# Performance work log

Measured on AMD Instinct MI355X. Metric: run time of the kernel, lower is better.

Reference implementation:

```python
import jax, jax.numpy as jnp
import numpy as np

NUM_HEADS = 6
DIM = 192
WIN = 7  # window_size = (7, 7), n = 49
N = WIN * WIN
TABLE = (2 * WIN - 1) * (2 * WIN - 1)  # 169
SCALE = (DIM // NUM_HEADS) ** (-0.5)


def setup_inputs() -> dict:
    key = jax.random.key(0)
    k1, k2, k3, k4, k5, k6 = jax.random.split(key, 6)
    B_ = 8192   # num_windows * batch = 1024 * 8
    NW = 1024   # windows per image (224/7)^2
    qkv = jax.random.normal(k1, (B_, N, 3 * DIM), dtype=jnp.float32)
    rpi = jax.random.randint(k2, (N, N), 0, TABLE, dtype=jnp.int64)
    # shift-window mask: 0 where attend, -100 where masked (Swin convention)
    mask = jnp.where(jax.random.uniform(k3, (NW, N, N)) < 0.8, 0.0, -100.0).astype(jnp.float32)
    bias_table = 0.02 * jax.random.normal(k4, (TABLE, NUM_HEADS), dtype=jnp.float32)
    proj_w = 0.02 * jax.random.normal(k5, (DIM, DIM), dtype=jnp.float32)
    proj_b = jnp.zeros((DIM,), dtype=jnp.float32)
    return {"qkv": qkv, "rpi": rpi, "mask": mask,
            "bias_table": bias_table, "proj_w": proj_w, "proj_b": proj_b}


def reference(qkv, rpi, mask, bias_table, proj_w, proj_b):
    b_, n, c3 = qkv.shape
    c = c3 // 3
    hd = c // NUM_HEADS
    # (b_, n, 3, h, hd) -> (3, b_, h, n, hd)
    qkv = qkv.reshape(b_, n, 3, NUM_HEADS, hd).transpose(2, 0, 3, 1, 4)
    q, k, v = qkv[0], qkv[1], qkv[2]
    attn = jnp.einsum('bhid,bhjd->bhij', q * SCALE, k)  # (b_, h, n, n)
    # relative position bias gather: (n*n,) -> (n, n, h) -> (h, n, n)
    rpb = bias_table[rpi.reshape(-1)].reshape(n, n, NUM_HEADS).transpose(2, 0, 1)
    attn = attn + rpb[None]
    nw = mask.shape[0]
    attn = attn.reshape(b_ // nw, nw, NUM_HEADS, n, n) + mask[None, :, None]
    attn = jax.nn.softmax(attn.reshape(b_, NUM_HEADS, n, n), axis=-1)
    x = jnp.einsum('bhij,bhjd->bhid', attn, v)          # (b_, h, n, hd)
    x = x.transpose(0, 2, 1, 3).reshape(b_, n, c)
    return x @ proj_w.T + proj_b
```

## Files before the change

kernel.cpp:

```cpp
#include <hip/hip_runtime.h>

#define NH 6
#define NTOK 49
#define CDIM 192
#define NWIN 1024
#define SCALE 0.17677669529663687f

typedef __bf16 bf16x8 __attribute__((ext_vector_type(8)));
typedef float f32x4 __attribute__((ext_vector_type(4)));
typedef unsigned short u16;
typedef unsigned int u32;

__device__ __forceinline__ u16 bfr(float x) { return __builtin_bit_cast(u16, (__bf16)x); }

__global__ void build_wb(const float* __restrict__ w, u16* __restrict__ wb) {
    int i = blockIdx.x * 256 + threadIdx.x;
    if (i < CDIM * CDIM) wb[i] = bfr(w[i]);
}

__global__ __launch_bounds__(256, 4)
void swin_fused(const float* __restrict__ qkv, const int* __restrict__ rpi,
                const float* __restrict__ mask, const float* __restrict__ bias_table,
                const u16* __restrict__ wb, const float* __restrict__ proj_b,
                float* __restrict__ out) {
    __shared__ u16 k_s[64][40];
    __shared__ u16 vT_s[32][72];
    __shared__ u16 p_s[64][72];

    const int tid = threadIdx.x;
    const int b = blockIdx.x;
    const int wn = b & (NWIN - 1);
    const int wv = tid >> 6;
    const int lane = tid & 63;
    const int lg = lane >> 4;
    const int lc = lane & 15;

    const float* qkvb = qkv + (size_t)b * (NTOK * 3 * CDIM);
    const float* mrow = mask + (size_t)wn * (NTOK * NTOK);
    const f32x4 fzero = {0.f, 0.f, 0.f, 0.f};

    const int n0 = tid >> 3, f0 = tid & 7;
    const bool s1 = tid < 136;
    const int n1 = (tid + 256) >> 3, f1 = (tid + 256) & 7;
    const float* kb0 = qkvb + n0 * 576 + CDIM + f0 * 4;
    const float* vb0 = qkvb + n0 * 576 + 2 * CDIM + f0 * 4;
    const float* kb1 = qkvb + n1 * 576 + CDIM + f1 * 4;
    const float* vb1 = qkvb + n1 * 576 + 2 * CDIM + f1 * 4;

    const int qrow = (16 * wv + lc < NTOK) ? 16 * wv + lc : NTOK - 1;
    const float* qptr = qkvb + (size_t)qrow * 576 + 8 * lg;

    float4 kp0 = *reinterpret_cast<const float4*>(kb0);
    float4 vp0 = *reinterpret_cast<const float4*>(vb0);
    float4 kp1 = {0, 0, 0, 0}, vp1 = {0, 0, 0, 0};
    if (s1) {
        kp1 = *reinterpret_cast<const float4*>(kb1);
        vp1 = *reinterpret_cast<const float4*>(vb1);
    }
    float4 qfA = *reinterpret_cast<const float4*>(qptr);
    float4 qfB = *reinterpret_cast<const float4*>(qptr + 4);

    u32 bidx2[8];
    u32 mbits = 0, vbits = 0;
#pragma unroll
    for (int r = 0; r < 4; ++r) {
        const int i = 16 * wv + 4 * lg + r;
#pragma unroll
        for (int t = 0; t < 4; ++t) {
            const int j = 16 * t + lc;
            const int idx = r * 4 + t;
            const bool valid = (i < NTOK) && (j < NTOK);
            const int ij = valid ? i * NTOK + j : 0;
            const u32 bi = (u32)(rpi[ij] * NH);
            if (idx & 1) bidx2[idx >> 1] |= bi << 16; else bidx2[idx >> 1] = bi;
            const float mv = valid ? mrow[ij] : 0.f;
            if (!valid) vbits |= 1u << idx;
            if (mv < -50.f) mbits |= 1u << idx;
        }
    }

    for (int idx = tid; idx < 512; idx += 256) {
        const int d = idx >> 4, m = idx & 15;
        if (m) vT_s[d][48 + m] = 0;
    }

    {
        ushort4 ko;
        ko.x = bfr(kp0.x); ko.y = bfr(kp0.y); ko.z = bfr(kp0.z); ko.w = bfr(kp0.w);
        *reinterpret_cast<ushort4*>(&k_s[n0][f0 * 4]) = ko;
        const int d0 = f0 * 4;
        vT_s[d0 + 0][n0] = bfr(vp0.x); vT_s[d0 + 1][n0] = bfr(vp0.y);
        vT_s[d0 + 2][n0] = bfr(vp0.z); vT_s[d0 + 3][n0] = bfr(vp0.w);
        if (s1) {
            ushort4 k1;
            k1.x = bfr(kp1.x); k1.y = bfr(kp1.y); k1.z = bfr(kp1.z); k1.w = bfr(kp1.w);
            *reinterpret_cast<ushort4*>(&k_s[n1][f1 * 4]) = k1;
            const int d1 = f1 * 4;
            vT_s[d1 + 0][n1] = bfr(vp1.x); vT_s[d1 + 1][n1] = bfr(vp1.y);
            vT_s[d1 + 2][n1] = bfr(vp1.z); vT_s[d1 + 3][n1] = bfr(vp1.w);
        }
    }
    __syncthreads();

    bf16x8 af[NH];

#pragma unroll
    for (int h = 0; h < NH; ++h) {
        if (h + 1 < NH) {
            kp0 = *reinterpret_cast<const float4*>(kb0 + (h + 1) * 32);
            vp0 = *reinterpret_cast<const float4*>(vb0 + (h + 1) * 32);
            if (s1) {
                kp1 = *reinterpret_cast<const float4*>(kb1 + (h + 1) * 32);
                vp1 = *reinterpret_cast<const float4*>(vb1 + (h + 1) * 32);
            }
        }

        bf16x8 aq;
        aq[0] = (__bf16)(qfA.x * SCALE); aq[1] = (__bf16)(qfA.y * SCALE);
        aq[2] = (__bf16)(qfA.z * SCALE); aq[3] = (__bf16)(qfA.w * SCALE);
        aq[4] = (__bf16)(qfB.x * SCALE); aq[5] = (__bf16)(qfB.y * SCALE);
        aq[6] = (__bf16)(qfB.z * SCALE); aq[7] = (__bf16)(qfB.w * SCALE);
        if (h + 1 < NH) {
            qfA = *reinterpret_cast<const float4*>(qptr + (h + 1) * 32);
            qfB = *reinterpret_cast<const float4*>(qptr + (h + 1) * 32 + 4);
        }

        bf16x8 bk[4];
#pragma unroll
        for (int t = 0; t < 4; ++t)
            bk[t] = *reinterpret_cast<const bf16x8*>(&k_s[16 * t + lc][8 * lg]);

        float bias_v[4][4];
#pragma unroll
        for (int r = 0; r < 4; ++r)
#pragma unroll
            for (int t = 0; t < 4; ++t) {
                const int idx = r * 4 + t;
                const u32 bp = bidx2[idx >> 1];
                const int bi = (idx & 1) ? (int)(bp >> 16) : (int)(bp & 0xFFFFu);
                bias_v[r][t] = bias_table[bi + h];
            }

        f32x4 acc[4];
#pragma unroll
        for (int t = 0; t < 4; ++t)
            acc[t] = __builtin_amdgcn_mfma_f32_16x16x32_bf16(aq, bk[t], fzero, 0, 0, 0);

#pragma unroll
        for (int r = 0; r < 4; ++r) {
            const int i = 16 * wv + 4 * lg + r;
            float vals[4];
#pragma unroll
            for (int t = 0; t < 4; ++t) {
                const int idx = r * 4 + t;
                float v = acc[t][r] + bias_v[r][t] + (((mbits >> idx) & 1u) ? -100.f : 0.f);
                vals[t] = ((vbits >> idx) & 1u) ? -1e30f : v;
            }
            float m = fmaxf(fmaxf(vals[0], vals[1]), fmaxf(vals[2], vals[3]));
#pragma unroll
            for (int off = 1; off < 16; off <<= 1) m = fmaxf(m, __shfl_xor(m, off, 16));
            float e[4], s = 0.f;
#pragma unroll
            for (int t = 0; t < 4; ++t) { e[t] = __expf(vals[t] - m); s += e[t]; }
#pragma unroll
            for (int off = 1; off < 16; off <<= 1) s += __shfl_xor(s, off, 16);
            const float rs = 1.0f / s;
#pragma unroll
            for (int t = 0; t < 4; ++t)
                p_s[i][16 * t + lc] = bfr(e[t] * rs);
        }

        f32x4 xacc[2] = {fzero, fzero};
#pragma unroll
        for (int ks = 0; ks < 2; ++ks) {
            const bf16x8 pa = *reinterpret_cast<const bf16x8*>(&p_s[16 * wv + lc][32 * ks + 8 * lg]);
#pragma unroll
            for (int ct = 0; ct < 2; ++ct) {
                const bf16x8 vv = *reinterpret_cast<const bf16x8*>(&vT_s[16 * ct + lc][32 * ks + 8 * lg]);
                xacc[ct] = __builtin_amdgcn_mfma_f32_16x16x32_bf16(pa, vv, xacc[ct], 0, 0, 0);
            }
        }

#pragma unroll
        for (int ct = 0; ct < 2; ++ct)
#pragma unroll
            for (int r = 0; r < 4; ++r)
                p_s[16 * wv + 4 * lg + r][16 * ct + lc] = bfr(xacc[ct][r]);
        af[h] = *reinterpret_cast<const bf16x8*>(&p_s[16 * wv + lc][8 * lg]);

        if (h + 1 < NH) {
            __syncthreads();
            ushort4 ko;
            ko.x = bfr(kp0.x); ko.y = bfr(kp0.y); ko.z = bfr(kp0.z); ko.w = bfr(kp0.w);
            *reinterpret_cast<ushort4*>(&k_s[n0][f0 * 4]) = ko;
            const int d0 = f0 * 4;
            vT_s[d0 + 0][n0] = bfr(vp0.x); vT_s[d0 + 1][n0] = bfr(vp0.y);
            vT_s[d0 + 2][n0] = bfr(vp0.z); vT_s[d0 + 3][n0] = bfr(vp0.w);
            if (s1) {
                ushort4 k1;
                k1.x = bfr(kp1.x); k1.y = bfr(kp1.y); k1.z = bfr(kp1.z); k1.w = bfr(kp1.w);
                *reinterpret_cast<ushort4*>(&k_s[n1][f1 * 4]) = k1;
                const int d1 = f1 * 4;
                vT_s[d1 + 0][n1] = bfr(vp1.x); vT_s[d1 + 1][n1] = bfr(vp1.y);
                vT_s[d1 + 2][n1] = bfr(vp1.z); vT_s[d1 + 3][n1] = bfr(vp1.w);
            }
            __syncthreads();
        }
    }

    f32x4 pacc[12];
#pragma unroll
    for (int ct = 0; ct < 12; ++ct) pacc[ct] = fzero;

#pragma unroll
    for (int ks = 0; ks < NH; ++ks) {
#pragma unroll
        for (int ct = 0; ct < 12; ++ct) {
            const bf16x8 bw = *reinterpret_cast<const bf16x8*>(wb + (16 * ct + lc) * CDIM + ks * 32 + 8 * lg);
            pacc[ct] = __builtin_amdgcn_mfma_f32_16x16x32_bf16(af[ks], bw, pacc[ct], 0, 0, 0);
        }
    }

#pragma unroll
    for (int ct = 0; ct < 12; ++ct) {
        const int c = 16 * ct + lc;
        const float pb = proj_b[c];
#pragma unroll
        for (int r = 0; r < 4; ++r) {
            const int i = 16 * wv + 4 * lg + r;
            if (i < NTOK)
                out[(size_t)b * (NTOK * CDIM) + i * CDIM + c] = pacc[ct][r] + pb;
        }
    }
}

extern "C" void kernel_launch(void* const* d_in, const int* in_sizes, int n_in,
                              void* d_out, int out_size, void* d_ws, size_t ws_size,
                              hipStream_t stream) {
    const float* qkv        = (const float*)d_in[0];
    const int*   rpi        = (const int*)d_in[1];
    const float* mask       = (const float*)d_in[2];
    const float* bias_table = (const float*)d_in[3];
    const float* proj_w     = (const float*)d_in[4];
    const float* proj_b     = (const float*)d_in[5];
    float* out = (float*)d_out;
    u16* wb = (u16*)d_ws;

    const int nblk = in_sizes[0] / (NTOK * 3 * CDIM);

    build_wb<<<(CDIM * CDIM + 255) / 256, 256, 0, stream>>>(proj_w, wb);
    swin_fused<<<nblk, 256, 0, stream>>>(qkv, rpi, mask, bias_table, wb, proj_b, out);
}
```

Baseline: 599.5 us.

## Transpose QK^T MFMA so each lane owns a full score row

```diff
diff --git a/kernel.cpp b/kernel.cpp
--- a/kernel.cpp
+++ b/kernel.cpp
@@ -60,28 +60,29 @@
     float4 qfA = *reinterpret_cast<const float4*>(qptr);
     float4 qfB = *reinterpret_cast<const float4*>(qptr + 4);
 
-    u32 bidx2[8];
-    u32 mbits = 0, vbits = 0;
-#pragma unroll
-    for (int r = 0; r < 4; ++r) {
-        const int i = 16 * wv + 4 * lg + r;
-#pragma unroll
-        for (int t = 0; t < 4; ++t) {
-            const int j = 16 * t + lc;
-            const int idx = r * 4 + t;
-            const bool valid = (i < NTOK) && (j < NTOK);
-            const int ij = valid ? i * NTOK + j : 0;
-            const u32 bi = (u32)(rpi[ij] * NH);
-            if (idx & 1) bidx2[idx >> 1] |= bi << 16; else bidx2[idx >> 1] = bi;
-            const float mv = valid ? mrow[ij] : 0.f;
-            if (!valid) vbits |= 1u << idx;
-            if (mv < -50.f) mbits |= 1u << idx;
-        }
+    int bofs[4][4];
+    float maddf[4][4];
+    {
+        const int i = 16 * wv + lc;
+#pragma unroll
+        for (int t = 0; t < 4; ++t)
+#pragma unroll
+            for (int r = 0; r < 4; ++r) {
+                const int j = 16 * t + 4 * lg + r;
+                const bool valid = (i < NTOK) && (j < NTOK);
+                const int ij = valid ? i * NTOK + j : 0;
+                bofs[t][r] = rpi[ij] * NH;
+                maddf[t][r] = valid ? mrow[ij] : -1e30f;
+            }
     }
 
     for (int idx = tid; idx < 512; idx += 256) {
         const int d = idx >> 4, m = idx & 15;
         if (m) vT_s[d][48 + m] = 0;
+    }
+    for (int idx = tid; idx < 600; idx += 256) {
+        const int rr = idx / 40, cc = idx % 40;
+        k_s[49 + rr][cc] = 0;
     }
 
     {
@@ -125,49 +126,59 @@
             qfB = *reinterpret_cast<const float4*>(qptr + (h + 1) * 32 + 4);
         }
 
+        float bias_v[4][4];
+#pragma unroll
+        for (int t = 0; t < 4; ++t)
+#pragma unroll
+            for (int r = 0; r < 4; ++r)
+                bias_v[t][r] = bias_table[bofs[t][r] + h];
+
         bf16x8 bk[4];
 #pragma unroll
         for (int t = 0; t < 4; ++t)
             bk[t] = *reinterpret_cast<const bf16x8*>(&k_s[16 * t + lc][8 * lg]);
-
-        float bias_v[4][4];
-#pragma unroll
-        for (int r = 0; r < 4; ++r)
+        f32x4 acc[4];
+#pragma unroll
+        for (int t = 0; t < 4; ++t)
+            acc[t] = __builtin_amdgcn_mfma_f32_16x16x32_bf16(bk[t], aq, fzero, 0, 0, 0);
+
+        float vals[4][4];
+#pragma unroll
+        for (int t = 0; t < 4; ++t)
+#pragma unroll
+            for (int r = 0; r < 4; ++r)
+                vals[t][r] = acc[t][r] + bias_v[t][r] + maddf[t][r];
+
+        float mx[4];
+#pragma unroll
+        for (int t = 0; t < 4; ++t)
+            mx[t] = fmaxf(fmaxf(vals[t][0], vals[t][1]), fmaxf(vals[t][2], vals[t][3]));
+        float m = fmaxf(fmaxf(mx[0], mx[1]), fmaxf(mx[2], mx[3]));
+        m = fmaxf(m, __shfl_xor(m, 16));
+        m = fmaxf(m, __shfl_xor(m, 32));
+
+        float e[4][4];
+        float s = 0.f;
+#pragma unroll
+        for (int t = 0; t < 4; ++t) {
+            float st = 0.f;
+#pragma unroll
+            for (int r = 0; r < 4; ++r) { e[t][r] = __expf(vals[t][r] - m); st += e[t][r]; }
+            s += st;
+        }
+        s += __shfl_xor(s, 16);
+        s += __shfl_xor(s, 32);
+        const float rs = 1.0f / s;
+
+        {
+            u16* prow = &p_s[16 * wv + lc][4 * lg];
 #pragma unroll
             for (int t = 0; t < 4; ++t) {
-                const int idx = r * 4 + t;
-                const u32 bp = bidx2[idx >> 1];
-                const int bi = (idx & 1) ? (int)(bp >> 16) : (int)(bp & 0xFFFFu);
-                bias_v[r][t] = bias_table[bi + h];
-            }
-
-        f32x4 acc[4];
-#pragma unroll
-        for (int t = 0; t < 4; ++t)
-            acc[t] = __builtin_amdgcn_mfma_f32_16x16x32_bf16(aq, bk[t], fzero, 0, 0, 0);
-
-#pragma unroll
-        for (int r = 0; r < 4; ++r) {
-            const int i = 16 * wv + 4 * lg + r;
-            float vals[4];
-#pragma unroll
-            for (int t = 0; t < 4; ++t) {
-                const int idx = r * 4 + t;
-                float v = acc[t][r] + bias_v[r][t] + (((mbits >> idx) & 1u) ? -100.f : 0.f);
-                vals[t] = ((vbits >> idx) & 1u) ? -1e30f : v;
-            }
-            float m = fmaxf(fmaxf(vals[0], vals[1]), fmaxf(vals[2], vals[3]));
-#pragma unroll
-            for (int off = 1; off < 16; off <<= 1) m = fmaxf(m, __shfl_xor(m, off, 16));
-            float e[4], s = 0.f;
-#pragma unroll
-            for (int t = 0; t < 4; ++t) { e[t] = __expf(vals[t] - m); s += e[t]; }
-#pragma unroll
-            for (int off = 1; off < 16; off <<= 1) s += __shfl_xor(s, off, 16);
-            const float rs = 1.0f / s;
-#pragma unroll
-            for (int t = 0; t < 4; ++t)
-                p_s[i][16 * t + lc] = bfr(e[t] * rs);
+                ushort4 pk;
+                pk.x = bfr(e[t][0] * rs); pk.y = bfr(e[t][1] * rs);
+                pk.z = bfr(e[t][2] * rs); pk.w = bfr(e[t][3] * rs);
+                *reinterpret_cast<ushort4*>(prow + 16 * t) = pk;
+            }
         }
 
         f32x4 xacc[2] = {fzero, fzero};
```

Result: faster. 561.4 us (-6.4%).
